# Kernel optimization log

Measured on AMD Instinct MI355X. Metric: run time of the kernel, lower is better.

The kernel has to match this reference:

```python
import jax, jax.numpy as jnp
import numpy as np

T, I, H, O = 8192, 512, 1024, 2


def setup_inputs() -> dict:
    key = jax.random.key(0)
    ks = jax.random.split(key, 7)
    s_ih = 1.0 / np.sqrt(H)
    return {
        "input_seq": jax.random.normal(ks[0], (T, I), dtype=jnp.float32),
        "W_ih": jax.random.normal(ks[1], (4 * H, I), dtype=jnp.float32) * s_ih,
        "W_hh": jax.random.normal(ks[2], (4 * H, H), dtype=jnp.float32) * s_ih,
        "b_ih": jax.random.normal(ks[3], (4 * H,), dtype=jnp.float32) * s_ih,
        "b_hh": jax.random.normal(ks[4], (4 * H,), dtype=jnp.float32) * s_ih,
        "W_lin": jax.random.normal(ks[5], (O, H), dtype=jnp.float32) * s_ih,
        "b_lin": jax.random.normal(ks[6], (O,), dtype=jnp.float32) * s_ih,
    }


def reference(input_seq, W_ih, W_hh, b_ih, b_hh, W_lin, b_lin):
    h0 = jnp.zeros((H,), dtype=input_seq.dtype)
    c0 = jnp.zeros((H,), dtype=input_seq.dtype)
    # Precompute input projections for all timesteps: (T, 4H)
    x_gates = input_seq @ W_ih.T + b_ih + b_hh

    def step(carry, xg):
        h, c = carry
        gates = xg + h @ W_hh.T  # (4H,) in PyTorch order i, f, g, o
        i_g, f_g, g_g, o_g = jnp.split(gates, 4)
        i_g = jax.nn.sigmoid(i_g)
        f_g = jax.nn.sigmoid(f_g)
        g_g = jnp.tanh(g_g)
        o_g = jax.nn.sigmoid(o_g)
        c_new = f_g * c + i_g * g_g
        h_new = o_g * jnp.tanh(c_new)
        return (h_new, c_new), h_new

    _, hs = jax.lax.scan(step, (h0, c0), x_gates)  # hs: (T, H)
    logits = hs @ W_lin.T + b_lin  # (T, O)
    return jax.nn.softmax(logits, axis=-1)
```

## Files before the change

kernel.cpp:

```cpp
#include <hip/hip_runtime.h>
#include <stdint.h>

#define T_STEPS 8192
#define IN_DIM  512
#define HID     1024
#define G4      4096
#define NBLK    64
#define NW      16

typedef unsigned long long u64;

__global__ __launch_bounds__(256) void gemm_xgates(
    const float* __restrict__ A,
    const float* __restrict__ W,
    const float* __restrict__ bih,
    const float* __restrict__ bhh,
    float* __restrict__ xg)
{
    __shared__ float At[8][128];
    __shared__ float Bt[8][128];
    const int tid = threadIdx.x;
    const int r0 = blockIdx.x * 128;
    const int t0 = blockIdx.y * 128;
    const int tx = tid & 15, ty = tid >> 4;
    const int lrow = tid >> 1;
    const int kq   = (tid & 1) * 4;

    float acc[8][8];
#pragma unroll
    for (int i = 0; i < 8; ++i)
#pragma unroll
        for (int j = 0; j < 8; ++j) acc[i][j] = 0.f;

    for (int k0 = 0; k0 < IN_DIM; k0 += 8) {
        float4 av = *(const float4*)&A[(size_t)(t0 + lrow) * IN_DIM + k0 + kq];
        float4 bv = *(const float4*)&W[(size_t)(r0 + lrow) * IN_DIM + k0 + kq];
        __syncthreads();
        At[kq + 0][lrow] = av.x; At[kq + 1][lrow] = av.y;
        At[kq + 2][lrow] = av.z; At[kq + 3][lrow] = av.w;
        Bt[kq + 0][lrow] = bv.x; Bt[kq + 1][lrow] = bv.y;
        Bt[kq + 2][lrow] = bv.z; Bt[kq + 3][lrow] = bv.w;
        __syncthreads();
#pragma unroll
        for (int k = 0; k < 8; ++k) {
            float4 a0 = *(const float4*)&At[k][ty * 8];
            float4 a1 = *(const float4*)&At[k][ty * 8 + 4];
            float4 b0 = *(const float4*)&Bt[k][tx * 8];
            float4 b1 = *(const float4*)&Bt[k][tx * 8 + 4];
            float aa[8] = {a0.x, a0.y, a0.z, a0.w, a1.x, a1.y, a1.z, a1.w};
            float bb[8] = {b0.x, b0.y, b0.z, b0.w, b1.x, b1.y, b1.z, b1.w};
#pragma unroll
            for (int i = 0; i < 8; ++i)
#pragma unroll
                for (int j = 0; j < 8; ++j) acc[i][j] += aa[i] * bb[j];
        }
    }

    float bias[8];
#pragma unroll
    for (int j = 0; j < 8; ++j) {
        int r = r0 + tx * 8 + j;
        bias[j] = bih[r] + bhh[r];
    }
#pragma unroll
    for (int i = 0; i < 8; ++i) {
        int t = t0 + ty * 8 + i;
        float4 o0 = make_float4(acc[i][0] + bias[0], acc[i][1] + bias[1],
                                acc[i][2] + bias[2], acc[i][3] + bias[3]);
        float4 o1 = make_float4(acc[i][4] + bias[4], acc[i][5] + bias[5],
                                acc[i][6] + bias[6], acc[i][7] + bias[7]);
        *(float4*)&xg[(size_t)t * G4 + r0 + tx * 8]     = o0;
        *(float4*)&xg[(size_t)t * G4 + r0 + tx * 8 + 4] = o1;
    }
}

__device__ __forceinline__ float sigm_f(float x) {
    return 1.f / (1.f + __expf(-x));
}
__device__ __forceinline__ float tanh_f(float x) {
    x = fminf(fmaxf(x, -15.f), 15.f);
    float e = __expf(2.f * x);
    return (e - 1.f) / (e + 1.f);
}

__device__ __forceinline__ float dpp_reduce_add(float x) {
    int v;
    v = __builtin_amdgcn_update_dpp(0, __float_as_int(x), 0x111, 0xf, 0xf, true);
    x += __int_as_float(v);
    v = __builtin_amdgcn_update_dpp(0, __float_as_int(x), 0x112, 0xf, 0xf, true);
    x += __int_as_float(v);
    v = __builtin_amdgcn_update_dpp(0, __float_as_int(x), 0x114, 0xf, 0xf, true);
    x += __int_as_float(v);
    v = __builtin_amdgcn_update_dpp(0, __float_as_int(x), 0x118, 0xf, 0xf, true);
    x += __int_as_float(v);
    v = __builtin_amdgcn_update_dpp(0, __float_as_int(x), 0x142, 0xa, 0xf, true);
    x += __int_as_float(v);
    v = __builtin_amdgcn_update_dpp(0, __float_as_int(x), 0x143, 0xc, 0xf, true);
    x += __int_as_float(v);
    return x;
}
__device__ __forceinline__ float lane63(float x) {
    return __uint_as_float(__builtin_amdgcn_readlane(__float_as_uint(x), 63));
}

__global__ __launch_bounds__(1024, 1) void lstm_rec(
    const float* __restrict__ Whh,
    const float* __restrict__ xg,
    float* __restrict__ hs,
    u64* __restrict__ hdata)
{
    __shared__ float2 hinp2[512];
    __shared__ float  hout[NW];

    const int tid = threadIdx.x;
    const int b   = blockIdx.x;
    const int w   = tid >> 6;
    const int l   = tid & 63;
    const int j   = b * NW + w;
    const int ju  = __builtin_amdgcn_readfirstlane(j);

    float2 wreg2[4][8];
#pragma unroll
    for (int s = 0; s < 4; ++s) {
        const float* row = &Whh[(size_t)(s * 1024 + j) * HID];
#pragma unroll
        for (int i = 0; i < 8; ++i) {
            wreg2[s][i].x = row[128 * i + l];
            wreg2[s][i].y = row[128 * i + 64 + l];
        }
    }
#pragma unroll
    for (int s = 0; s < 4; ++s)
#pragma unroll
        for (int i = 0; i < 8; ++i) {
            asm volatile("" : "+v"(wreg2[s][i].x));
            asm volatile("" : "+v"(wreg2[s][i].y));
        }

    float xv[4];
#pragma unroll
    for (int s = 0; s < 4; ++s)
        xv[s] = xg[(size_t)0 * G4 + s * 1024 + ju];

    float c = 0.f;

    for (int t = 0; t < T_STEPS; ++t) {
        if (t > 0 && w < 4) {
            const u64* base = hdata + (((size_t)(t - 1) & 1) << 10) + 256 * w;
            const u64 want = (u64)(uint32_t)t;
            u64 v0, v1, v2, v3;
            for (;;) {
                v0 = __hip_atomic_load(base + l,       __ATOMIC_RELAXED, __HIP_MEMORY_SCOPE_AGENT);
                v1 = __hip_atomic_load(base + 64 + l,  __ATOMIC_RELAXED, __HIP_MEMORY_SCOPE_AGENT);
                v2 = __hip_atomic_load(base + 128 + l, __ATOMIC_RELAXED, __HIP_MEMORY_SCOPE_AGENT);
                v3 = __hip_atomic_load(base + 192 + l, __ATOMIC_RELAXED, __HIP_MEMORY_SCOPE_AGENT);
                bool ok = ((v0 >> 32) == want) & ((v1 >> 32) == want) &
                          ((v2 >> 32) == want) & ((v3 >> 32) == want);
                if (__all(ok)) break;
            }
            hinp2[128 * w + l] = make_float2(__uint_as_float((uint32_t)v0),
                                             __uint_as_float((uint32_t)v1));
            hinp2[128 * w + 64 + l] = make_float2(__uint_as_float((uint32_t)v2),
                                                  __uint_as_float((uint32_t)v3));
        }
        __syncthreads();

        float2 hval2[8];
        if (t > 0) {
#pragma unroll
            for (int i = 0; i < 8; ++i) hval2[i] = hinp2[64 * i + l];
        } else {
#pragma unroll
            for (int i = 0; i < 8; ++i) hval2[i] = make_float2(0.f, 0.f);
        }

        float xn[4] = {0.f, 0.f, 0.f, 0.f};
        if (t < T_STEPS - 1) {
#pragma unroll
            for (int s = 0; s < 4; ++s)
                xn[s] = xg[(size_t)(t + 1) * G4 + s * 1024 + ju];
        }

        float gsum[4];
#pragma unroll
        for (int s = 0; s < 4; ++s) {
            float2 a2 = make_float2(0.f, 0.f);
#pragma unroll
            for (int i = 0; i < 8; ++i) {
                a2.x = fmaf(wreg2[s][i].x, hval2[i].x, a2.x);
                a2.y = fmaf(wreg2[s][i].y, hval2[i].y, a2.y);
            }
            gsum[s] = lane63(dpp_reduce_add(a2.x + a2.y));
        }

        float ig = sigm_f(xv[0] + gsum[0]);
        float fg = sigm_f(xv[1] + gsum[1]);
        float gv = tanh_f(xv[2] + gsum[2]);
        float og = sigm_f(xv[3] + gsum[3]);
        c = fg * c + ig * gv;
        float h = og * tanh_f(c);

        if (l == 0) hout[w] = h;
        __syncthreads();

        if (w == 0 && l < NW) {
            float hv = hout[l];
            hs[(size_t)(t + 1) * HID + b * NW + l] = hv;
            u64 pub = ((u64)(uint32_t)(t + 1) << 32) | (u64)__float_as_uint(hv);
            __hip_atomic_store(&hdata[(((size_t)t & 1) << 10) + b * NW + l], pub,
                               __ATOMIC_RELAXED, __HIP_MEMORY_SCOPE_AGENT);
        }

#pragma unroll
        for (int s = 0; s < 4; ++s) xv[s] = xn[s];
    }
}

__global__ __launch_bounds__(256) void proj_softmax(
    const float* __restrict__ hs,
    const float* __restrict__ Wl,
    const float* __restrict__ bl,
    float* __restrict__ out)
{
    const int tid = threadIdx.x;
    const int w = tid >> 6, l = tid & 63;
    const int row = blockIdx.x * 4 + w;
    const float* h = &hs[(size_t)(row + 1) * HID];

    float a0 = 0.f, a1 = 0.f;
#pragma unroll
    for (int i = 0; i < 4; ++i) {
        float4 hv = *(const float4*)&h[256 * i + 4 * l];
        float4 w0 = *(const float4*)&Wl[256 * i + 4 * l];
        float4 w1 = *(const float4*)&Wl[HID + 256 * i + 4 * l];
        a0 = fmaf(hv.x, w0.x, a0); a0 = fmaf(hv.y, w0.y, a0);
        a0 = fmaf(hv.z, w0.z, a0); a0 = fmaf(hv.w, w0.w, a0);
        a1 = fmaf(hv.x, w1.x, a1); a1 = fmaf(hv.y, w1.y, a1);
        a1 = fmaf(hv.z, w1.z, a1); a1 = fmaf(hv.w, w1.w, a1);
    }
#pragma unroll
    for (int off = 1; off < 64; off <<= 1) {
        a0 += __shfl_xor(a0, off, 64);
        a1 += __shfl_xor(a1, off, 64);
    }
    if (l == 0) {
        float l0 = a0 + bl[0];
        float l1 = a1 + bl[1];
        float m  = fmaxf(l0, l1);
        float e0 = __expf(l0 - m), e1 = __expf(l1 - m);
        float inv = 1.f / (e0 + e1);
        float2 o = make_float2(e0 * inv, e1 * inv);
        *(float2*)&out[(size_t)row * 2] = o;
    }
}

extern "C" void kernel_launch(void* const* d_in, const int* in_sizes, int n_in,
                              void* d_out, int out_size, void* d_ws, size_t ws_size,
                              hipStream_t stream)
{
    const float* input = (const float*)d_in[0];
    const float* W_ih  = (const float*)d_in[1];
    const float* W_hh  = (const float*)d_in[2];
    const float* b_ih  = (const float*)d_in[3];
    const float* b_hh  = (const float*)d_in[4];
    const float* W_lin = (const float*)d_in[5];
    const float* b_lin = (const float*)d_in[6];
    float* out = (float*)d_out;

    char* ws = (char*)d_ws;
    float* hs     = (float*)ws;
    size_t hs_b   = (size_t)(T_STEPS + 1) * HID * sizeof(float);
    u64*   hdata  = (u64*)(ws + hs_b);
    size_t hd_b   = 2 * 1024 * sizeof(u64);
    float* xg     = (float*)(ws + hs_b + hd_b);


    dim3 g1(G4 / 128, T_STEPS / 128);
    gemm_xgates<<<g1, 256, 0, stream>>>(input, W_ih, b_ih, b_hh, xg);

    lstm_rec<<<NBLK, NW * 64, 0, stream>>>(W_hh, xg, hs, hdata);

    proj_softmax<<<T_STEPS / 4, 256, 0, stream>>>(hs, W_lin, b_lin, out);
}
```

Baseline: 20.50 ms.

## Spread h polling across all waves and publish per-wave without second barrier

Every one of the 16 waves now polls its own 64-entry slice of the published hidden state, where before four waves each polled 256 entries. Each wave publishes its own h from lane 63 directly to global memory, which removes the shared-memory staging and the second __syncthreads per timestep. The dot product uses one accumulator over 16 scalar weights instead of paired float2 accumulators, and the readlane broadcast is dropped because only lane 63 consumes the result. This shortens the serial critical path per step, at the cost of more concurrent polling traffic and a single FMA dependency chain.

```diff
diff --git a/kernel.cpp b/kernel.cpp
--- a/kernel.cpp
+++ b/kernel.cpp
@@ -99,9 +99,6 @@
     x += __int_as_float(v);
     return x;
 }
-__device__ __forceinline__ float lane63(float x) {
-    return __uint_as_float(__builtin_amdgcn_readlane(__float_as_uint(x), 63));
-}
 
 __global__ __launch_bounds__(1024, 1) void lstm_rec(
     const float* __restrict__ Whh,
@@ -109,8 +106,7 @@
     float* __restrict__ hs,
     u64* __restrict__ hdata)
 {
-    __shared__ float2 hinp2[512];
-    __shared__ float  hout[NW];
+    __shared__ float hinp[HID];
 
     const int tid = threadIdx.x;
     const int b   = blockIdx.x;
@@ -119,23 +115,18 @@
     const int j   = b * NW + w;
     const int ju  = __builtin_amdgcn_readfirstlane(j);
 
-    float2 wreg2[4][8];
+    float wreg[4][16];
 #pragma unroll
     for (int s = 0; s < 4; ++s) {
         const float* row = &Whh[(size_t)(s * 1024 + j) * HID];
 #pragma unroll
-        for (int i = 0; i < 8; ++i) {
-            wreg2[s][i].x = row[128 * i + l];
-            wreg2[s][i].y = row[128 * i + 64 + l];
-        }
+        for (int i = 0; i < 16; ++i) wreg[s][i] = row[64 * i + l];
     }
 #pragma unroll
     for (int s = 0; s < 4; ++s)
 #pragma unroll
-        for (int i = 0; i < 8; ++i) {
-            asm volatile("" : "+v"(wreg2[s][i].x));
-            asm volatile("" : "+v"(wreg2[s][i].y));
-        }
+        for (int i = 0; i < 16; ++i)
+            asm volatile("" : "+v"(wreg[s][i]));
 
     float xv[4];
 #pragma unroll
@@ -145,33 +136,26 @@
     float c = 0.f;
 
     for (int t = 0; t < T_STEPS; ++t) {
-        if (t > 0 && w < 4) {
-            const u64* base = hdata + (((size_t)(t - 1) & 1) << 10) + 256 * w;
-            const u64 want = (u64)(uint32_t)t;
-            u64 v0, v1, v2, v3;
+        if (t > 0) {
+            const u64* base = hdata + (((size_t)(t - 1) & 1) << 10) + 64 * w;
+            const uint32_t want32 = (uint32_t)t;
+            u64 v;
             for (;;) {
-                v0 = __hip_atomic_load(base + l,       __ATOMIC_RELAXED, __HIP_MEMORY_SCOPE_AGENT);
-                v1 = __hip_atomic_load(base + 64 + l,  __ATOMIC_RELAXED, __HIP_MEMORY_SCOPE_AGENT);
-                v2 = __hip_atomic_load(base + 128 + l, __ATOMIC_RELAXED, __HIP_MEMORY_SCOPE_AGENT);
-                v3 = __hip_atomic_load(base + 192 + l, __ATOMIC_RELAXED, __HIP_MEMORY_SCOPE_AGENT);
-                bool ok = ((v0 >> 32) == want) & ((v1 >> 32) == want) &
-                          ((v2 >> 32) == want) & ((v3 >> 32) == want);
-                if (__all(ok)) break;
+                v = __hip_atomic_load(base + l, __ATOMIC_RELAXED,
+                                      __HIP_MEMORY_SCOPE_AGENT);
+                if (__all((uint32_t)(v >> 32) == want32)) break;
             }
-            hinp2[128 * w + l] = make_float2(__uint_as_float((uint32_t)v0),
-                                             __uint_as_float((uint32_t)v1));
-            hinp2[128 * w + 64 + l] = make_float2(__uint_as_float((uint32_t)v2),
-                                                  __uint_as_float((uint32_t)v3));
+            hinp[64 * w + l] = __uint_as_float((uint32_t)v);
         }
         __syncthreads();
 
-        float2 hval2[8];
+        float hval[16];
         if (t > 0) {
 #pragma unroll
-            for (int i = 0; i < 8; ++i) hval2[i] = hinp2[64 * i + l];
+            for (int i = 0; i < 16; ++i) hval[i] = hinp[64 * i + l];
         } else {
 #pragma unroll
-            for (int i = 0; i < 8; ++i) hval2[i] = make_float2(0.f, 0.f);
+            for (int i = 0; i < 16; ++i) hval[i] = 0.f;
         }
 
         float xn[4] = {0.f, 0.f, 0.f, 0.f};
@@ -184,13 +168,10 @@
         float gsum[4];
 #pragma unroll
         for (int s = 0; s < 4; ++s) {
-            float2 a2 = make_float2(0.f, 0.f);
-#pragma unroll
-            for (int i = 0; i < 8; ++i) {
-                a2.x = fmaf(wreg2[s][i].x, hval2[i].x, a2.x);
-                a2.y = fmaf(wreg2[s][i].y, hval2[i].y, a2.y);
-            }
-            gsum[s] = lane63(dpp_reduce_add(a2.x + a2.y));
+            float a = 0.f;
+#pragma unroll
+            for (int i = 0; i < 16; ++i) a = fmaf(wreg[s][i], hval[i], a);
+            gsum[s] = dpp_reduce_add(a);
         }
 
         float ig = sigm_f(xv[0] + gsum[0]);
@@ -200,14 +181,10 @@
         c = fg * c + ig * gv;
         float h = og * tanh_f(c);
 
-        if (l == 0) hout[w] = h;
-        __syncthreads();
-
-        if (w == 0 && l < NW) {
-            float hv = hout[l];
-            hs[(size_t)(t + 1) * HID + b * NW + l] = hv;
-            u64 pub = ((u64)(uint32_t)(t + 1) << 32) | (u64)__float_as_uint(hv);
-            __hip_atomic_store(&hdata[(((size_t)t & 1) << 10) + b * NW + l], pub,
+        if (l == 63) {
+            hs[(size_t)(t + 1) * HID + j] = h;
+            u64 pub = ((u64)(uint32_t)(t + 1) << 32) | (u64)__float_as_uint(h);
+            __hip_atomic_store(&hdata[(((size_t)t & 1) << 10) + j], pub,
                                __ATOMIC_RELAXED, __HIP_MEMORY_SCOPE_AGENT);
         }
 
```

Result: slower. 26.04 ms (+27.1%).

## Replace second per-step barrier with LDS tag flags and double-buffered h input

Applied to the files above, without the earlier changes.

The persistent LSTM recurrence drops the second __syncthreads per timestep. Each wave now writes its h value plus a release-tagged flag to LDS, and wave 4 spins on those flags before publishing h globally. The LDS h input buffer is double-buffered so a fast wave cannot overwrite data still being read. The readlane after the DPP reduction is removed and the divisions in sigmoid and tanh become hardware reciprocals. This cuts per-step synchronisation latency on the serial critical path, at the cost of spin-wait traffic and correctness that depends on DPP lane-63 semantics and LDS memory ordering.

```diff
diff --git a/kernel.cpp b/kernel.cpp
--- a/kernel.cpp
+++ b/kernel.cpp
@@ -75,12 +75,12 @@
 }
 
 __device__ __forceinline__ float sigm_f(float x) {
-    return 1.f / (1.f + __expf(-x));
+    return __builtin_amdgcn_rcpf(1.f + __expf(-x));
 }
 __device__ __forceinline__ float tanh_f(float x) {
     x = fminf(fmaxf(x, -15.f), 15.f);
     float e = __expf(2.f * x);
-    return (e - 1.f) / (e + 1.f);
+    return (e - 1.f) * __builtin_amdgcn_rcpf(e + 1.f);
 }
 
 __device__ __forceinline__ float dpp_reduce_add(float x) {
@@ -98,9 +98,6 @@
     v = __builtin_amdgcn_update_dpp(0, __float_as_int(x), 0x143, 0xc, 0xf, true);
     x += __int_as_float(v);
     return x;
-}
-__device__ __forceinline__ float lane63(float x) {
-    return __uint_as_float(__builtin_amdgcn_readlane(__float_as_uint(x), 63));
 }
 
 __global__ __launch_bounds__(1024, 1) void lstm_rec(
@@ -109,8 +106,9 @@
     float* __restrict__ hs,
     u64* __restrict__ hdata)
 {
-    __shared__ float2 hinp2[512];
-    __shared__ float  hout[NW];
+    __shared__ float2   hinp2[2][512];
+    __shared__ float    hout_h[NW];
+    __shared__ uint32_t hout_tag[NW];
 
     const int tid = threadIdx.x;
     const int b   = blockIdx.x;
@@ -119,6 +117,8 @@
     const int j   = b * NW + w;
     const int ju  = __builtin_amdgcn_readfirstlane(j);
 
+    if (tid < NW) hout_tag[tid] = 0;
+
     float2 wreg2[4][8];
 #pragma unroll
     for (int s = 0; s < 4; ++s) {
@@ -145,6 +145,7 @@
     float c = 0.f;
 
     for (int t = 0; t < T_STEPS; ++t) {
+        const int buf = t & 1;
         if (t > 0 && w < 4) {
             const u64* base = hdata + (((size_t)(t - 1) & 1) << 10) + 256 * w;
             const u64 want = (u64)(uint32_t)t;
@@ -158,17 +159,17 @@
                           ((v2 >> 32) == want) & ((v3 >> 32) == want);
                 if (__all(ok)) break;
             }
-            hinp2[128 * w + l] = make_float2(__uint_as_float((uint32_t)v0),
-                                             __uint_as_float((uint32_t)v1));
-            hinp2[128 * w + 64 + l] = make_float2(__uint_as_float((uint32_t)v2),
-                                                  __uint_as_float((uint32_t)v3));
+            hinp2[buf][128 * w + l] = make_float2(__uint_as_float((uint32_t)v0),
+                                                  __uint_as_float((uint32_t)v1));
+            hinp2[buf][128 * w + 64 + l] = make_float2(__uint_as_float((uint32_t)v2),
+                                                       __uint_as_float((uint32_t)v3));
         }
         __syncthreads();
 
         float2 hval2[8];
         if (t > 0) {
 #pragma unroll
-            for (int i = 0; i < 8; ++i) hval2[i] = hinp2[64 * i + l];
+            for (int i = 0; i < 8; ++i) hval2[i] = hinp2[buf][64 * i + l];
         } else {
 #pragma unroll
             for (int i = 0; i < 8; ++i) hval2[i] = make_float2(0.f, 0.f);
@@ -190,7 +191,7 @@
                 a2.x = fmaf(wreg2[s][i].x, hval2[i].x, a2.x);
                 a2.y = fmaf(wreg2[s][i].y, hval2[i].y, a2.y);
             }
-            gsum[s] = lane63(dpp_reduce_add(a2.x + a2.y));
+            gsum[s] = dpp_reduce_add(a2.x + a2.y);
         }
 
         float ig = sigm_f(xv[0] + gsum[0]);
@@ -200,15 +201,28 @@
         c = fg * c + ig * gv;
         float h = og * tanh_f(c);
 
-        if (l == 0) hout[w] = h;
-        __syncthreads();
-
-        if (w == 0 && l < NW) {
-            float hv = hout[l];
-            hs[(size_t)(t + 1) * HID + b * NW + l] = hv;
-            u64 pub = ((u64)(uint32_t)(t + 1) << 32) | (u64)__float_as_uint(hv);
-            __hip_atomic_store(&hdata[(((size_t)t & 1) << 10) + b * NW + l], pub,
-                               __ATOMIC_RELAXED, __HIP_MEMORY_SCOPE_AGENT);
+        if (l == 63) {
+            hout_h[w] = h;
+            __hip_atomic_store(&hout_tag[w], (uint32_t)(t + 1),
+                               __ATOMIC_RELEASE, __HIP_MEMORY_SCOPE_WORKGROUP);
+        }
+
+        if (w == 4) {
+            const uint32_t want = (uint32_t)(t + 1);
+            for (;;) {
+                uint32_t tg = (l < NW)
+                    ? __hip_atomic_load(&hout_tag[l], __ATOMIC_ACQUIRE,
+                                        __HIP_MEMORY_SCOPE_WORKGROUP)
+                    : want;
+                if (__all(tg == want)) break;
+            }
+            if (l < NW) {
+                float hv = hout_h[l];
+                u64 pub = ((u64)want << 32) | (u64)__float_as_uint(hv);
+                __hip_atomic_store(&hdata[((size_t)buf << 10) + b * NW + l], pub,
+                                   __ATOMIC_RELAXED, __HIP_MEMORY_SCOPE_AGENT);
+                hs[(size_t)(t + 1) * HID + b * NW + l] = hv;
+            }
         }
 
 #pragma unroll
```

Result: faster. 18.12 ms (-11.6%).
